# Performance work log

Measured on AMD Instinct MI355X. Metric: run time of the kernel, lower is better.

Reference implementation:

```python
import jax, jax.numpy as jnp
import numpy as np

B, NF, L, DEPTH = 128, 1781, 2048, 4
DI, DS, DC, DTR = 8, 32, 4, 1  # d_inner=expand*d_model, d_state, d_conv, dt_rank


def setup_inputs() -> dict:
    key = jax.random.key(0)
    ks = jax.random.split(key, 32)
    n = lambda k, s, sc=0.02: jax.random.normal(k, s, jnp.float32) * sc
    inp = {
        'x': jax.random.normal(ks[0], (B, NF), jnp.float32),
        # projection1: ReLU -> Linear(NF,2048) -> LayerNorm(2048)
        'p1_W': n(ks[1], (L, NF)), 'p1_b': jnp.zeros((L,), jnp.float32),
        'ln1_g': jnp.ones((L,), jnp.float32), 'ln1_b': jnp.zeros((L,), jnp.float32),
        # per-block Mamba params stacked over depth
        'in_W': n(ks[2], (DEPTH, 2 * DI, 1)),
        'conv_w': n(ks[3], (DEPTH, DI, 1, DC), 0.2),
        'conv_b': jnp.zeros((DEPTH, DI), jnp.float32),
        'xp_W': n(ks[4], (DEPTH, DTR + 2 * DS, DI)),
        'dt_W': n(ks[5], (DEPTH, DI, DTR), 0.5),
        'dt_b': n(ks[6], (DEPTH, DI), 0.5) - 4.0,
        'A_log': jnp.log(jnp.tile(jnp.arange(1, DS + 1, dtype=jnp.float32), (DEPTH, DI, 1))),
        'Dp': jnp.ones((DEPTH, DI), jnp.float32),
        'out_W': n(ks[7], (DEPTH, 1, DI)),
        'rms_w': jnp.ones((DEPTH, 1), jnp.float32),
        # projection2: Linear(2048,512) -> LayerNorm(512) -> ReLU -> Linear(512,256)
        'p2a_W': n(ks[8], (512, L)), 'p2a_b': jnp.zeros((512,), jnp.float32),
        'ln2_g': jnp.ones((512,), jnp.float32), 'ln2_b': jnp.zeros((512,), jnp.float32),
        'p2b_W': n(ks[9], (256, 512)), 'p2b_b': jnp.zeros((256,), jnp.float32),
    }
    return inp


def _layernorm(x, g, b, eps=1e-5):
    m = x.mean(-1, keepdims=True)
    v = ((x - m) ** 2).mean(-1, keepdims=True)
    return (x - m) * jax.lax.rsqrt(v + eps) * g + b


def _silu(x):
    return x * jax.nn.sigmoid(x)


def _mamba(x, in_W, conv_w, conv_b, xp_W, dt_W, dt_b, A_log, Dp, out_W):
    # x: (B, L, 1)
    xz = x @ in_W.T                      # (B, L, 2*DI)
    xc, z = jnp.split(xz, 2, axis=-1)    # (B, L, DI) each
    # causal depthwise conv over L
    xt = jnp.transpose(xc, (0, 2, 1))    # (B, DI, L)
    xt = jax.lax.conv_general_dilated(xt, conv_w, (1,), [(DC - 1, 0)],
                                      dimension_numbers=('NCH', 'OIH', 'NCH'),
                                      feature_group_count=DI)
    xc = _silu(jnp.transpose(xt, (0, 2, 1)) + conv_b)   # (B, L, DI)
    x_dbl = xc @ xp_W.T                                  # (B, L, DTR+2*DS)
    dt, Bm, Cm = jnp.split(x_dbl, [DTR, DTR + DS], axis=-1)
    dt = jax.nn.softplus(dt @ dt_W.T + dt_b)             # (B, L, DI)
    A = -jnp.exp(A_log)                                  # (DI, DS)
    dA = jnp.exp(dt[..., None] * A)                      # (B, L, DI, DS)
    dBx = dt[..., None] * Bm[:, :, None, :] * xc[..., None]
    def comb(e1, e2):
        a1, b1 = e1
        a2, b2 = e2
        return (a2 * a1, a2 * b1 + b2)
    _, h = jax.lax.associative_scan(comb, (dA, dBx), axis=1)  # h: (B,L,DI,DS)
    y = jnp.einsum('blds,bls->bld', h, Cm) + Dp * xc
    y = y * _silu(z)
    return y @ out_W.T                                   # (B, L, 1)


def reference(x, p1_W, p1_b, ln1_g, ln1_b, in_W, conv_w, conv_b, xp_W, dt_W, dt_b,
              A_log, Dp, out_W, rms_w, p2a_W, p2a_b, ln2_g, ln2_b, p2b_W, p2b_b):
    h = jax.nn.relu(x) @ p1_W.T + p1_b
    h = _layernorm(h, ln1_g, ln1_b)
    h = h[..., None]                      # (B, L, 1)
    for i in range(DEPTH):
        # RMSNorm over last dim (size 1): mean(x^2) == x^2
        rn = h * jax.lax.rsqrt(h * h + 1e-5) * rms_w[i]
        h = _mamba(rn, in_W[i], conv_w[i], conv_b[i], xp_W[i], dt_W[i], dt_b[i],
                   A_log[i], Dp[i], out_W[i]) + h
    h = h[..., 0]
    h2 = h @ p2a_W.T + p2a_b
    h2 = jax.nn.relu(_layernorm(h2, ln2_g, ln2_b))
    return h2 @ p2b_W.T + p2b_b
```

## Files before the change

kernel.cpp:

```cpp
#include <hip/hip_runtime.h>
#include <math.h>

#define B_    128
#define NF_   1781
#define L_    2048
#define DEPTH_ 4
#define DI_   8
#define DS_   32
#define NXD_  65
#define NCC_  8
#define CLL_  256
#define SUB_  32
#define MCL_  64
#define KS1_  8
#define KS3_  8
#define LOG2E_ 1.44269504088896f

typedef unsigned long long ull_t;
union F2U { float2 f; ull_t u; };

__device__ __forceinline__ float silu_f(float x) {
    return x / (1.f + __expf(-x));
}
__device__ __forceinline__ float softplus_f(float x) {
    return fmaxf(x, 0.f) + __logf(1.f + __expf(-fabsf(x)));
}
__device__ __forceinline__ float exp2_fast(float x) {
#if __has_builtin(__builtin_amdgcn_exp2f)
    return __builtin_amdgcn_exp2f(x);
#else
    return __expf(x * 0.6931471805599453f);
#endif
}

#define DPP_ADD(x, ctrl)                                                      \
    (x) += __int_as_float(__builtin_amdgcn_update_dpp(                        \
        0, __float_as_int(x), (ctrl), 0xf, 0xf, true))

__device__ __forceinline__ float dpp_sum32_tail(float x) {
    DPP_ADD(x, 0x111);
    DPP_ADD(x, 0x112);
    DPP_ADD(x, 0x114);
    DPP_ADD(x, 0x118);
    DPP_ADD(x, 0x142);
    return x;
}

__device__ __forceinline__ float wave_sum64(float v) {
    v += __shfl_xor(v, 32); v += __shfl_xor(v, 16); v += __shfl_xor(v, 8);
    v += __shfl_xor(v, 4);  v += __shfl_xor(v, 2);  v += __shfl_xor(v, 1);
    return v;
}

__device__ __forceinline__ float block_sum256(float v, float* red) {
    v = wave_sum64(v);
    int tid = threadIdx.x;
    __syncthreads();
    if ((tid & 63) == 0) red[tid >> 6] = v;
    __syncthreads();
    return red[0] + red[1] + red[2] + red[3];
}

__global__ __launch_bounds__(256) void kZero(float4* __restrict__ p) {
    p[blockIdx.x * 256 + threadIdx.x] = make_float4(0.f, 0.f, 0.f, 0.f);
}

__global__ __launch_bounds__(256) void kZeroCtl(unsigned int* __restrict__ p,
                                                int n) {
    int i = blockIdx.x * 256 + threadIdx.x;
    if (i < n) p[i] = 0u;
}

__global__ __launch_bounds__(256) void k1_gemm(const float* __restrict__ x,
                                               const float* __restrict__ W,
                                               float* __restrict__ g1) {
    __shared__ float As[32][36];
    __shared__ float Bs[32][65];
    const int n0 = blockIdx.x * 64, m0 = blockIdx.y * 32;
    const int kb = blockIdx.z * 224;
    const int tid = threadIdx.x;
    const int tn = tid & 63, tm = tid >> 6;
    float acc[8] = {0.f, 0.f, 0.f, 0.f, 0.f, 0.f, 0.f, 0.f};
#pragma unroll 1
    for (int t = 0; t < 7; ++t) {
        const int k0 = kb + t * 32;
#pragma unroll
        for (int j = 0; j < 4; ++j) {
            int idx = tid + 256 * j, k = idx & 31, m = idx >> 5;
            int kk = k0 + k;
            float v = (kk < NF_) ? x[(m0 + m) * NF_ + kk] : 0.f;
            As[k][m] = fmaxf(v, 0.f);
        }
#pragma unroll
        for (int j = 0; j < 8; ++j) {
            int idx = tid + 256 * j, k = idx & 31, n = idx >> 5;
            int kk = k0 + k;
            Bs[k][n] = (kk < NF_) ? W[(size_t)(n0 + n) * NF_ + kk] : 0.f;
        }
        __syncthreads();
#pragma unroll
        for (int k = 0; k < 32; ++k) {
            float4 a0 = *(const float4*)&As[k][tm * 8];
            float4 a1 = *(const float4*)&As[k][tm * 8 + 4];
            float b0 = Bs[k][tn];
            acc[0] = fmaf(a0.x, b0, acc[0]); acc[1] = fmaf(a0.y, b0, acc[1]);
            acc[2] = fmaf(a0.z, b0, acc[2]); acc[3] = fmaf(a0.w, b0, acc[3]);
            acc[4] = fmaf(a1.x, b0, acc[4]); acc[5] = fmaf(a1.y, b0, acc[5]);
            acc[6] = fmaf(a1.z, b0, acc[6]); acc[7] = fmaf(a1.w, b0, acc[7]);
        }
        __syncthreads();
    }
#pragma unroll
    for (int r = 0; r < 8; ++r)
        atomicAdd(&g1[(m0 + tm * 8 + r) * L_ + n0 + tn], acc[r]);
}

__global__ __launch_bounds__(256) void kLN(float* __restrict__ hg,
                                           const float* __restrict__ bias,
                                           const float* __restrict__ g,
                                           const float* __restrict__ bt) {
    __shared__ float red[4];
    const int tid = threadIdx.x;
    float* h = hg + blockIdx.x * L_;
    float s = 0.f;
    for (int l = tid; l < L_; l += 256) s += h[l] + bias[l];
    s = block_sum256(s, red);
    const float mean = s * (1.f / (float)L_);
    float vs = 0.f;
    for (int l = tid; l < L_; l += 256) {
        float d = h[l] + bias[l] - mean; vs += d * d;
    }
    vs = block_sum256(vs, red);
    const float rstd = rsqrtf(vs * (1.f / (float)L_) + 1e-5f);
    for (int l = tid; l < L_; l += 256)
        h[l] = (h[l] + bias[l] - mean) * rstd * g[l] + bt[l];
}

__global__ __launch_bounds__(256) void kS(int dep,
    float* __restrict__ hg, ull_t* __restrict__ PSa,
    unsigned int* __restrict__ ctl,
    const float* __restrict__ in_W,  const float* __restrict__ conv_w,
    const float* __restrict__ conv_b,const float* __restrict__ xp_W,
    const float* __restrict__ dt_W,  const float* __restrict__ dt_b,
    const float* __restrict__ A_log, const float* __restrict__ Dp,
    const float* __restrict__ out_W, const float* __restrict__ rms_w) {
    __shared__ float rnb[CLL_ + 3];
    __shared__ float Pp[88];
    __shared__ float xcvb[CLL_ * 8];
    __shared__ float dtS[CLL_ * 8];
    __shared__ float2 bufA[(SUB_ / 2) * 32];
    __shared__ float2 bufB[(SUB_ / 2) * 32];
    __shared__ float ypartS[SUB_ * 9];
    __shared__ int svid;
    unsigned int* flags  = ctl;
    unsigned int* ticket = ctl + B_ * NCC_;
    const int tid = threadIdx.x;
    if (tid == 0) svid = (int)atomicAdd(&ticket[dep], 1u);
    __syncthreads();
    const int vid = svid;
    const int b = vid >> 3, c = vid & (NCC_ - 1);
    const int c0 = c * CLL_;

    {
        const float rmsw = rms_w[dep];
        for (int i = tid; i < CLL_ + 3; i += 256) {
            int lg = c0 - 3 + i;
            float hv = (lg >= 0) ? hg[(size_t)b * L_ + lg] : 0.f;
            rnb[i] = (lg >= 0) ? hv * rsqrtf(hv * hv + 1e-5f) * rmsw : 0.f;
        }
        if (tid < 88) {
            int t2 = tid;
            Pp[t2] = (t2 < 32)  ? conv_w[dep * 32 + t2]
                   : (t2 < 40)  ? conv_b[dep * 8 + t2 - 32]
                   : (t2 < 56)  ? in_W[dep * 16 + t2 - 40]
                   : (t2 < 64)  ? dt_W[dep * 8 + t2 - 56]
                   : (t2 < 72)  ? dt_b[dep * 8 + t2 - 64]
                   : (t2 < 80)  ? Dp[dep * 8 + t2 - 72]
                                : out_W[dep * 8 + t2 - 80];
        }
    }
    __syncthreads();

    {
        const int dd = tid & 7, lb = tid >> 3;
        const float cw0 = Pp[dd * 4], cw1 = Pp[dd * 4 + 1];
        const float cw2 = Pp[dd * 4 + 2], cw3 = Pp[dd * 4 + 3];
        const float inw = Pp[40 + dd], cb = Pp[32 + dd];
        const float xp0d = xp_W[dep * (NXD_ * 8) + dd];
        const float dtw = Pp[56 + dd], dtb = Pp[64 + dd];
#pragma unroll
        for (int jj = 0; jj < CLL_ / 32; ++jj) {
            int l = lb + 32 * jj;
            float sc = cw0 * rnb[l] + cw1 * rnb[l + 1] +
                       cw2 * rnb[l + 2] + cw3 * rnb[l + 3];
            float v = silu_f(inw * sc + cb);
            xcvb[l * 8 + dd] = v;
            float p = v * xp0d;
            DPP_ADD(p, 0x111); DPP_ADD(p, 0x112); DPP_ADD(p, 0x114);
            float dtraw = __shfl(p, tid | 7);
            dtS[l * 8 + dd] = softplus_f(dtraw * dtw + dtb);
        }
    }
    __syncthreads();

    const int d = tid >> 5, s = tid & 31;
    const int wave = tid >> 6, lane = tid & 63;
    const int kk = lane & 31, half = lane >> 5;
    const float AthL2 = -__expf(A_log[(dep * 8 + d) * 32 + s]) * LOG2E_;

    const float4* wpB = (const float4*)(xp_W + dep * (NXD_ * 8) + (kk + 1) * 8);
    const float4 wBa = wpB[0], wBb = wpB[1];
#define GEMV_B(t, buf)                                                        \
    {                                                                         \
        _Pragma("unroll")                                                     \
        for (int i = 0; i < 4; ++i) {                                         \
            int lsub = wave * 8 + half * 4 + i;                               \
            int l = (t) * SUB_ + lsub;                                        \
            float4 xa = *(const float4*)&xcvb[l * 8];                         \
            float4 xb = *(const float4*)&xcvb[l * 8 + 4];                     \
            float dot = xa.x * wBa.x + xa.y * wBa.y + xa.z * wBa.z +          \
                        xa.w * wBa.w + xb.x * wBb.x + xb.y * wBb.y +          \
                        xb.z * wBb.z + xb.w * wBb.w;                          \
            ((float*)&(buf)[(lsub >> 1) * 32 + kk])[lsub & 1] = dot;          \
        }                                                                     \
    }

    float hloc = 0.f, sdt = 0.f;
    GEMV_B(0, bufA)
    __syncthreads();
#pragma unroll 1
    for (int t = 0; t < CLL_ / SUB_; ++t) {
        if (t + 1 < CLL_ / SUB_) {
            if (t & 1) { GEMV_B(t + 1, bufA) } else { GEMV_B(t + 1, bufB) }
        }
        const float2* cur = (t & 1) ? bufB : bufA;
#pragma unroll
        for (int l2 = 0; l2 < SUB_ / 2; ++l2) {
            float2 bm = cur[l2 * 32 + s];
            int l = t * SUB_ + l2 * 2;
            float dtl = dtS[l * 8 + d];
            float dA = exp2_fast(dtl * AthL2);
            hloc = fmaf(dA, hloc, dtl * xcvb[l * 8 + d] * bm.x);
            sdt += dtl;
            dtl = dtS[(l + 1) * 8 + d];
            dA = exp2_fast(dtl * AthL2);
            hloc = fmaf(dA, hloc, dtl * xcvb[(l + 1) * 8 + d] * bm.y);
            sdt += dtl;
        }
        __syncthreads();
    }
    const float cp = exp2_fast(sdt * AthL2);

    const unsigned int want = (unsigned int)(dep + 1);
    if (c < NCC_ - 1) {
        F2U ou; ou.f = make_float2(cp, hloc);
        __hip_atomic_store(&PSa[((size_t)vid << 8) + tid], ou.u,
                           __ATOMIC_RELAXED, __HIP_MEMORY_SCOPE_AGENT);
    }
    __syncthreads();
    if (c < NCC_ - 1 && tid == 0)
        __hip_atomic_store(&flags[vid], want, __ATOMIC_RELAXED,
                           __HIP_MEMORY_SCOPE_AGENT);

    float h_in = 0.f;
    if (c > 0) {
        if (tid < c) {
            while (__hip_atomic_load(&flags[vid - c + tid], __ATOMIC_RELAXED,
                                     __HIP_MEMORY_SCOPE_AGENT) != want)
                __builtin_amdgcn_s_sleep(4);
        }
        __syncthreads();
        const ull_t* base = PSa + (((size_t)(vid - c)) << 8) + tid;
        ull_t tmp[NCC_ - 1];
#pragma unroll
        for (int j = 0; j < NCC_ - 1; ++j)
            if (j < c)
                tmp[j] = __hip_atomic_load(base + ((size_t)j << 8),
                                           __ATOMIC_RELAXED,
                                           __HIP_MEMORY_SCOPE_AGENT);
#pragma unroll
        for (int j = 0; j < NCC_ - 1; ++j)
            if (j < c) {
                F2U pu; pu.u = tmp[j];
                h_in = fmaf(pu.f.x, h_in, pu.f.y);
            }
    }

    const float4* wpC = (const float4*)(xp_W + dep * (NXD_ * 8) + (lane + 1) * 8);
    const float4 wCa = wpC[0], wCb = wpC[1];
#define GEMV_BC(t)                                                            \
    {                                                                         \
        _Pragma("unroll")                                                     \
        for (int i = 0; i < 8; ++i) {                                         \
            int lsub = wave * 8 + i;                                          \
            int l = (t) * SUB_ + lsub;                                        \
            float4 xa = *(const float4*)&xcvb[l * 8];                         \
            float4 xb = *(const float4*)&xcvb[l * 8 + 4];                     \
            float dot = xa.x * wCa.x + xa.y * wCa.y + xa.z * wCa.z +          \
                        xa.w * wCa.w + xb.x * wCb.x + xb.y * wCb.y +          \
                        xb.z * wCb.z + xb.w * wCb.w;                          \
            if (lane < 32)                                                    \
                ((float*)&bufA[(lsub >> 1) * 32 + kk])[lsub & 1] = dot;       \
            else                                                              \
                ((float*)&bufB[(lsub >> 1) * 32 + kk])[lsub & 1] = dot;       \
        }                                                                     \
    }

#define EPI(t)                                                                \
    if (tid < SUB_) {                                                         \
        int lg = (t) * SUB_ + tid;                                            \
        const float rv = rnb[3 + lg];                                         \
        float o = 0.f;                                                        \
        _Pragma("unroll")                                                     \
        for (int d2 = 0; d2 < 8; ++d2) {                                      \
            float wz = silu_f(rv * Pp[48 + d2]) * Pp[80 + d2];                \
            o += wz * (ypartS[tid * 9 + d2] +                                 \
                       Pp[72 + d2] * xcvb[lg * 8 + d2]);                      \
        }                                                                     \
        hg[(size_t)b * L_ + c0 + lg] += o;                                    \
    }

    float hst = h_in;
#pragma unroll 1
    for (int t = 0; t < CLL_ / SUB_; ++t) {
        GEMV_BC(t)
        if (t > 0) { EPI(t - 1) }
        __syncthreads();
#pragma unroll
        for (int l4 = 0; l4 < SUB_ / 4; ++l4) {
            int lbase = t * SUB_ + l4 * 4;
            float2 bm0 = bufA[(l4 * 2) * 32 + s];
            float2 bm1 = bufA[(l4 * 2 + 1) * 32 + s];
            float2 cm0 = bufB[(l4 * 2) * 32 + s];
            float2 cm1 = bufB[(l4 * 2 + 1) * 32 + s];
            float cr[4];
            float dtl = dtS[lbase * 8 + d];
            float dA = exp2_fast(dtl * AthL2);
            hst = fmaf(dA, hst, dtl * xcvb[lbase * 8 + d] * bm0.x);
            cr[0] = hst * cm0.x;
            dtl = dtS[(lbase + 1) * 8 + d];
            dA = exp2_fast(dtl * AthL2);
            hst = fmaf(dA, hst, dtl * xcvb[(lbase + 1) * 8 + d] * bm0.y);
            cr[1] = hst * cm0.y;
            dtl = dtS[(lbase + 2) * 8 + d];
            dA = exp2_fast(dtl * AthL2);
            hst = fmaf(dA, hst, dtl * xcvb[(lbase + 2) * 8 + d] * bm1.x);
            cr[2] = hst * cm1.x;
            dtl = dtS[(lbase + 3) * 8 + d];
            dA = exp2_fast(dtl * AthL2);
            hst = fmaf(dA, hst, dtl * xcvb[(lbase + 3) * 8 + d] * bm1.y);
            cr[3] = hst * cm1.y;
#pragma unroll
            for (int q = 0; q < 4; ++q) cr[q] = dpp_sum32_tail(cr[q]);
            if ((tid & 31) == 31) {
#pragma unroll
                for (int q = 0; q < 4; ++q)
                    ypartS[(l4 * 4 + q) * 9 + d] = cr[q];
            }
        }
        __syncthreads();
    }
    EPI(CLL_ / SUB_ - 1)
#undef GEMV_B
#undef GEMV_BC
#undef EPI
}

__global__ __launch_bounds__(256) void k3_gemm(const float* __restrict__ h,
                                               const float* __restrict__ W,
                                               float* __restrict__ part) {
    __shared__ float As[32][20];
    __shared__ float Bs[32][65];
    const int n0 = blockIdx.x * 64, m0 = blockIdx.y * 16;
    const int kb = blockIdx.z * 256;
    const int tid = threadIdx.x;
    const int tn = tid & 63, tm = tid >> 6;
    float acc[4] = {0.f, 0.f, 0.f, 0.f};
#pragma unroll 1
    for (int t = 0; t < 8; ++t) {
        const int k0 = kb + t * 32;
#pragma unroll
        for (int j = 0; j < 2; ++j) {
            int idx = tid + 256 * j, k = idx & 31, m = idx >> 5;
            As[k][m] = h[(m0 + m) * L_ + k0 + k];
        }
#pragma unroll
        for (int j = 0; j < 8; ++j) {
            int idx = tid + 256 * j, k = idx & 31, n = idx >> 5;
            Bs[k][n] = W[(size_t)(n0 + n) * L_ + k0 + k];
        }
        __syncthreads();
#pragma unroll
        for (int k = 0; k < 32; ++k) {
            float4 a = *(const float4*)&As[k][tm * 4];
            float b0 = Bs[k][tn];
            acc[0] = fmaf(a.x, b0, acc[0]);
            acc[1] = fmaf(a.y, b0, acc[1]);
            acc[2] = fmaf(a.z, b0, acc[2]);
            acc[3] = fmaf(a.w, b0, acc[3]);
        }
        __syncthreads();
    }
    float* pp = part + (size_t)blockIdx.z * (B_ * 512);
#pragma unroll
    for (int r = 0; r < 4; ++r)
        pp[(m0 + tm * 4 + r) * 512 + n0 + tn] = acc[r];
}

__global__ __launch_bounds__(256) void k4_head(const float* __restrict__ part,
    const float* __restrict__ b1,
    const float* __restrict__ g,  const float* __restrict__ bt,
    const float* __restrict__ W2, const float* __restrict__ b2,
    float* __restrict__ out) {
    __shared__ alignas(16) float t2r[512];
    __shared__ alignas(16) float y2[512];
    __shared__ float red[4];
    const int m = blockIdx.x, tid = threadIdx.x;
#pragma unroll
    for (int j = 0; j < 2; ++j) {
        const int n = tid + 256 * j;
        float v = b1[n];
#pragma unroll
        for (int ks = 0; ks < KS3_; ++ks)
            v += part[(size_t)ks * (B_ * 512) + m * 512 + n];
        t2r[n] = v;
    }
    __syncthreads();
    float v0 = t2r[tid], v1 = t2r[tid + 256];
    float s = block_sum256(v0 + v1, red);
    float mean = s * (1.f / 512.f);
    float d0 = v0 - mean, d1 = v1 - mean;
    float var = block_sum256(d0 * d0 + d1 * d1, red) * (1.f / 512.f);
    float rs = rsqrtf(var + 1e-5f);
    y2[tid]       = fmaxf(d0 * rs * g[tid] + bt[tid], 0.f);
    y2[tid + 256] = fmaxf(d1 * rs * g[tid + 256] + bt[tid + 256], 0.f);
    __syncthreads();
    float acc = b2[tid];
    const float* wr = W2 + tid * 512;
    for (int j = 0; j < 512; j += 4) {
        float4 w4 = *(const float4*)&wr[j];
        float4 yv = *(const float4*)&y2[j];
        acc = fmaf(w4.x, yv.x, acc); acc = fmaf(w4.y, yv.y, acc);
        acc = fmaf(w4.z, yv.z, acc); acc = fmaf(w4.w, yv.w, acc);
    }
    out[m * 256 + tid] = acc;
}

struct MambaLds {
    float P_in[16], P_cw[32], P_cb[8], P_dtw[8], P_dtb[8], P_dp[8], P_ow[8];
    alignas(16) float P_xp[NXD_ * 8];
    float rnb[L_ + 3];
    alignas(16) float xcvb[MCL_ * 8];
    alignas(16) float BmS[MCL_ * 33];
    alignas(16) float CmS[MCL_ * 33];
    float2 dtuS[MCL_ * 8];
    float dtrawS[MCL_], offS[MCL_];
    float ypartS[MCL_ * 8];
    float red[4];
};

__device__ void head_body(const float* hrow, float* t2r, float* y2, float* red,
    const float* __restrict__ W1, const float* __restrict__ b1,
    const float* __restrict__ g,  const float* __restrict__ bt,
    const float* __restrict__ W2, const float* __restrict__ b2,
    float* __restrict__ outrow) {
    const int tid = threadIdx.x, wave = tid >> 6, lane = tid & 63;
    for (int i = 0; i < 128; ++i) {
        const int n = wave * 128 + i;
        const float* wr = W1 + (size_t)n * L_;
        float acc = 0.f;
        for (int k0 = lane * 4; k0 < L_; k0 += 256) {
            float4 w4 = *(const float4*)&wr[k0];
            float4 hv = *(const float4*)&hrow[k0];
            acc = fmaf(w4.x, hv.x, acc); acc = fmaf(w4.y, hv.y, acc);
            acc = fmaf(w4.z, hv.z, acc); acc = fmaf(w4.w, hv.w, acc);
        }
        acc = wave_sum64(acc);
        if (lane == 0) t2r[n] = acc + b1[n];
    }
    __syncthreads();
    float v0 = t2r[tid], v1 = t2r[tid + 256];
    float s = block_sum256(v0 + v1, red);
    float mean = s * (1.f / 512.f);
    float d0 = v0 - mean, d1 = v1 - mean;
    float var = block_sum256(d0 * d0 + d1 * d1, red) * (1.f / 512.f);
    float rs = rsqrtf(var + 1e-5f);
    y2[tid]       = fmaxf(d0 * rs * g[tid] + bt[tid], 0.f);
    y2[tid + 256] = fmaxf(d1 * rs * g[tid + 256] + bt[tid + 256], 0.f);
    __syncthreads();
    for (int i = 0; i < 64; ++i) {
        const int n = wave * 64 + i;
        const float* wr = W2 + n * 512;
        float acc = 0.f;
        for (int k0 = lane * 4; k0 < 512; k0 += 256) {
            float4 w4 = *(const float4*)&wr[k0];
            float4 yv = *(const float4*)&y2[k0];
            acc = fmaf(w4.x, yv.x, acc); acc = fmaf(w4.y, yv.y, acc);
            acc = fmaf(w4.z, yv.z, acc); acc = fmaf(w4.w, yv.w, acc);
        }
        acc = wave_sum64(acc);
        if (lane == 0) outrow[n] = acc + b2[n];
    }
}

__device__ void mamba_body(float* h, MambaLds& S,
    const float* __restrict__ ln1_g, const float* __restrict__ ln1_b,
    const float* __restrict__ in_W,  const float* __restrict__ conv_w,
    const float* __restrict__ conv_b,const float* __restrict__ xp_W,
    const float* __restrict__ dt_W,  const float* __restrict__ dt_b,
    const float* __restrict__ A_log, const float* __restrict__ Dp,
    const float* __restrict__ out_W, const float* __restrict__ rms_w) {
    const int tid = threadIdx.x;
    float s = 0.f;
    for (int l = tid; l < L_; l += 256) s += h[l];
    s = block_sum256(s, S.red);
    const float mean = s * (1.f / (float)L_);
    float vs = 0.f;
    for (int l = tid; l < L_; l += 256) { float d = h[l] - mean; vs += d * d; }
    vs = block_sum256(vs, S.red);
    const float rstd = rsqrtf(vs * (1.f / (float)L_) + 1e-5f);
    for (int l = tid; l < L_; l += 256)
        h[l] = (h[l] - mean) * rstd * ln1_g[l] + ln1_b[l];
    __syncthreads();
    const int dd_s = tid >> 5, ss_s = tid & 31;
    for (int dep = 0; dep < DEPTH_; ++dep) {
        if (tid < 16) S.P_in[tid] = in_W[dep * 16 + tid];
        if (tid >= 32 && tid < 64) S.P_cw[tid - 32] = conv_w[dep * 32 + (tid - 32)];
        if (tid >= 64 && tid < 72) S.P_cb[tid - 64] = conv_b[dep * 8 + (tid - 64)];
        if (tid >= 72 && tid < 80) S.P_dtw[tid - 72] = dt_W[dep * 8 + (tid - 72)];
        if (tid >= 80 && tid < 88) S.P_dtb[tid - 80] = dt_b[dep * 8 + (tid - 80)];
        if (tid >= 88 && tid < 96) S.P_dp[tid - 88] = Dp[dep * 8 + (tid - 88)];
        if (tid >= 96 && tid < 104) S.P_ow[tid - 96] = out_W[dep * 8 + (tid - 96)];
        for (int j = tid; j < NXD_ * 8; j += 256) S.P_xp[j] = xp_W[dep * NXD_ * 8 + j];
        const float rmsw = rms_w[dep];
        const float Ath = -__expf(A_log[(dep * 8 + dd_s) * 32 + ss_s]);
        if (tid < 3) S.rnb[tid] = 0.f;
        __syncthreads();
        for (int l = tid; l < L_; l += 256) {
            float hv = h[l];
            S.rnb[3 + l] = hv * rsqrtf(hv * hv + 1e-5f) * rmsw;
        }
        __syncthreads();
        float hst = 0.f;
        for (int c0 = 0; c0 < L_; c0 += MCL_) {
            {
                const int dd = tid & 7, lb = tid >> 3;
                const float cw0 = S.P_cw[dd * 4 + 0], cw1 = S.P_cw[dd * 4 + 1];
                const float cw2 = S.P_cw[dd * 4 + 2], cw3 = S.P_cw[dd * 4 + 3];
                const float inw = S.P_in[dd], cb = S.P_cb[dd];
#pragma unroll
                for (int j = 0; j < MCL_ / 32; ++j) {
                    int l = lb + 32 * j, lg = c0 + l;
                    float sc = cw0 * S.rnb[lg] + cw1 * S.rnb[lg + 1] +
                               cw2 * S.rnb[lg + 2] + cw3 * S.rnb[lg + 3];
                    S.xcvb[l * 8 + dd] = silu_f(inw * sc + cb);
                }
            }
            __syncthreads();
            {
                const int l = tid & 63, q = tid >> 6;
                const float4 xa = *(const float4*)&S.xcvb[l * 8];
                const float4 xb = *(const float4*)&S.xcvb[l * 8 + 4];
                const int j0 = (q == 0) ? 0 : (17 + (q - 1) * 16);
                const int j1 = 17 + q * 16;
                for (int j = j0; j < j1; ++j) {
                    const float4 wa = *(const float4*)&S.P_xp[j * 8];
                    const float4 wb = *(const float4*)&S.P_xp[j * 8 + 4];
                    float dot = xa.x * wa.x + xa.y * wa.y + xa.z * wa.z + xa.w * wa.w +
                                xb.x * wb.x + xb.y * wb.y + xb.z * wb.z + xb.w * wb.w;
                    if (j == 0)      S.dtrawS[l] = dot;
                    else if (j < 33) S.BmS[l * 33 + (j - 1)] = dot;
                    else             S.CmS[l * 33 + (j - 33)] = dot;
                }
            }
            __syncthreads();
            {
                const int dd = tid & 7, lb = tid >> 3;
                const float dtw = S.P_dtw[dd], dtbv = S.P_dtb[dd];
#pragma unroll
                for (int j = 0; j < MCL_ / 32; ++j) {
                    int l = lb + 32 * j;
                    float dt = softplus_f(S.dtrawS[l] * dtw + dtbv);
                    float xcv = S.xcvb[l * 8 + dd];
                    S.dtuS[l * 8 + dd] = make_float2(dt, dt * xcv);
                }
            }
            if (tid < MCL_) {
                const int l = tid;
                const float rv = S.rnb[3 + c0 + l];
                float o = 0.f;
#pragma unroll
                for (int d2 = 0; d2 < 8; ++d2) {
                    float wz = silu_f(rv * S.P_in[8 + d2]) * S.P_ow[d2];
                    o += wz * S.P_dp[d2] * S.xcvb[l * 8 + d2];
                }
                S.offS[l] = o;
            }
            __syncthreads();
#pragma unroll 4
            for (int l = 0; l < MCL_; ++l) {
                float2 du = S.dtuS[l * 8 + dd_s];
                float Bv = S.BmS[l * 33 + ss_s];
                float Cv = S.CmS[l * 33 + ss_s];
                float dA = __expf(du.x * Ath);
                hst = fmaf(dA, hst, du.y * Bv);
                float c = dpp_sum32_tail(hst * Cv);
                if ((tid & 31) == 31) S.ypartS[l * 8 + dd_s] = c;
            }
            __syncthreads();
            if (tid < MCL_) {
                const int l = tid, lg = c0 + l;
                const float rv = S.rnb[3 + lg];
                float o = S.offS[l];
#pragma unroll
                for (int d2 = 0; d2 < 8; ++d2) {
                    float wz = silu_f(rv * S.P_in[8 + d2]) * S.P_ow[d2];
                    o += wz * S.ypartS[l * 8 + d2];
                }
                h[lg] += o;
            }
            __syncthreads();
        }
        __syncthreads();
    }
}

__global__ __launch_bounds__(256) void mega(
    const float* __restrict__ x,
    const float* __restrict__ p1_W, const float* __restrict__ p1_b,
    const float* __restrict__ ln1_g, const float* __restrict__ ln1_b,
    const float* __restrict__ in_W, const float* __restrict__ conv_w,
    const float* __restrict__ conv_b, const float* __restrict__ xp_W,
    const float* __restrict__ dt_W, const float* __restrict__ dt_b,
    const float* __restrict__ A_log, const float* __restrict__ Dp,
    const float* __restrict__ out_W, const float* __restrict__ rms_w,
    const float* __restrict__ p2a_W, const float* __restrict__ p2a_b,
    const float* __restrict__ ln2_g, const float* __restrict__ ln2_b,
    const float* __restrict__ p2b_W, const float* __restrict__ p2b_b,
    float* __restrict__ out) {
    __shared__ alignas(16) float hrow[L_];
    __shared__ MambaLds S;
    const int b = blockIdx.x, tid = threadIdx.x, wave = tid >> 6, lane = tid & 63;
    float* xrow = (float*)S.BmS;
    for (int k = tid; k < 1792; k += 256)
        xrow[k] = (k < NF_) ? fmaxf(x[b * NF_ + k], 0.f) : 0.f;
    __syncthreads();
    for (int i = 0; i < 512; ++i) {
        const int l = wave * 512 + i;
        const float* wr = p1_W + (size_t)l * NF_;
        float acc = 0.f;
        for (int k0 = lane * 4; k0 < NF_; k0 += 256) {
            if (k0 + 3 < NF_) {
                float4 w4 = *(const float4*)&wr[k0];
                float4 xv = *(const float4*)&xrow[k0];
                acc = fmaf(w4.x, xv.x, acc); acc = fmaf(w4.y, xv.y, acc);
                acc = fmaf(w4.z, xv.z, acc); acc = fmaf(w4.w, xv.w, acc);
            } else {
                for (int c = 0; c < 4; ++c)
                    if (k0 + c < NF_) acc = fmaf(wr[k0 + c], xrow[k0 + c], acc);
            }
        }
        acc = wave_sum64(acc);
        if (lane == 0) hrow[l] = acc + p1_b[l];
    }
    __syncthreads();
    mamba_body((float*)hrow, S, ln1_g, ln1_b, in_W, conv_w, conv_b,
               xp_W, dt_W, dt_b, A_log, Dp, out_W, rms_w);
    float* t2r = (float*)S.BmS;
    float* y2  = (float*)S.CmS;
    head_body((const float*)hrow, t2r, y2, S.red, p2a_W, p2a_b,
              ln2_g, ln2_b, p2b_W, p2b_b, out + b * 256);
}

extern "C" void kernel_launch(void* const* d_in, const int* in_sizes, int n_in,
                              void* d_out, int out_size, void* d_ws, size_t ws_size,
                              hipStream_t stream) {
    const float* x     = (const float*)d_in[0];
    const float* p1_W  = (const float*)d_in[1];
    const float* p1_b  = (const float*)d_in[2];
    const float* ln1_g = (const float*)d_in[3];
    const float* ln1_b = (const float*)d_in[4];
    const float* in_W  = (const float*)d_in[5];
    const float* conv_w= (const float*)d_in[6];
    const float* conv_b= (const float*)d_in[7];
    const float* xp_W  = (const float*)d_in[8];
    const float* dt_W  = (const float*)d_in[9];
    const float* dt_b  = (const float*)d_in[10];
    const float* A_log = (const float*)d_in[11];
    const float* Dp    = (const float*)d_in[12];
    const float* out_W = (const float*)d_in[13];
    const float* rms_w = (const float*)d_in[14];
    const float* p2a_W = (const float*)d_in[15];
    const float* p2a_b = (const float*)d_in[16];
    const float* ln2_g = (const float*)d_in[17];
    const float* ln2_b = (const float*)d_in[18];
    const float* p2b_W = (const float*)d_in[19];
    const float* p2b_b = (const float*)d_in[20];
    float* o = (float*)d_out;

    const size_t need = (size_t)B_ * L_ * sizeof(float);
    if (ws_size >= need) {
        float* h = (float*)d_ws;
        float* scr = (float*)d_in[1];
        ull_t* PSa = (ull_t*)scr;
        unsigned int* ctl = (unsigned int*)(scr + (size_t)B_ * NCC_ * 256 * 2);
        float* t2p = scr;

        kZero<<<L_ * B_ / 1024, 256, 0, stream>>>((float4*)h);
        dim3 grd1(L_ / 64, B_ / 32, KS1_);
        k1_gemm<<<grd1, 256, 0, stream>>>(x, p1_W, h);
        kZeroCtl<<<(B_ * NCC_ + DEPTH_ + 255) / 256, 256, 0, stream>>>(
            ctl, B_ * NCC_ + DEPTH_);
        kLN<<<B_, 256, 0, stream>>>(h, p1_b, ln1_g, ln1_b);
        for (int dep = 0; dep < DEPTH_; ++dep) {
            kS<<<dim3(B_ * NCC_), 256, 0, stream>>>(dep, h, PSa, ctl,
                                                    in_W, conv_w, conv_b, xp_W,
                                                    dt_W, dt_b, A_log, Dp,
                                                    out_W, rms_w);
        }
        dim3 grd3(512 / 64, B_ / 16, KS3_);
        k3_gemm<<<grd3, 256, 0, stream>>>(h, p2a_W, t2p);
        k4_head<<<B_, 256, 0, stream>>>(t2p, p2a_b, ln2_g, ln2_b,
                                        p2b_W, p2b_b, o);
    } else {
        mega<<<B_, 256, 0, stream>>>(x, p1_W, p1_b, ln1_g, ln1_b, in_W, conv_w,
                                     conv_b, xp_W, dt_W, dt_b, A_log, Dp, out_W,
                                     rms_w, p2a_W, p2a_b, ln2_g, ln2_b,
                                     p2b_W, p2b_b, o);
    }
}
```

Measured before the change: 471.1 us.

## Fuse four Mamba depth launches into one persistent kernel with halo exchange

Replaces the four per-depth scan kernel launches with a single kernel that loops over depth. Each chunk keeps its slice of the residual stream in shared memory, and only the 3-element conv halo goes through global memory to the next chunk, guarded by per-depth flags. This removes three launches, the global read-modify-write of h at every depth, and the wait at each kernel boundary, so chunks can move on to the next depth as soon as their left neighbour is ready. In exchange it needs more scratch space for per-depth prefix states and halos, and it relies on the ticket ordering to keep inter-block spin waits free of deadlock.

```diff
diff --git a/kernel.cpp b/kernel.cpp
--- a/kernel.cpp
+++ b/kernel.cpp
@@ -10,6 +10,7 @@
 #define NXD_  65
 #define NCC_  8
 #define CLL_  256
+#define NVID_ (B_ * NCC_)
 #define SUB_  32
 #define MCL_  64
 #define KS1_  8
@@ -136,14 +137,15 @@
         h[l] = (h[l] + bias[l] - mean) * rstd * g[l] + bt[l];
 }
 
-__global__ __launch_bounds__(256) void kS(int dep,
+__global__ __launch_bounds__(256) void kSF(
     float* __restrict__ hg, ull_t* __restrict__ PSa,
-    unsigned int* __restrict__ ctl,
+    float* __restrict__ halo, unsigned int* __restrict__ ctl,
     const float* __restrict__ in_W,  const float* __restrict__ conv_w,
     const float* __restrict__ conv_b,const float* __restrict__ xp_W,
     const float* __restrict__ dt_W,  const float* __restrict__ dt_b,
     const float* __restrict__ A_log, const float* __restrict__ Dp,
     const float* __restrict__ out_W, const float* __restrict__ rms_w) {
+    __shared__ float hS[CLL_];
     __shared__ float rnb[CLL_ + 3];
     __shared__ float Pp[88];
     __shared__ float xcvb[CLL_ * 8];
@@ -153,20 +155,49 @@
     __shared__ float ypartS[SUB_ * 9];
     __shared__ int svid;
     unsigned int* flags  = ctl;
-    unsigned int* ticket = ctl + B_ * NCC_;
+    unsigned int* eflags = ctl + NVID_;
+    unsigned int* ticket = ctl + 2 * NVID_;
     const int tid = threadIdx.x;
-    if (tid == 0) svid = (int)atomicAdd(&ticket[dep], 1u);
+    if (tid == 0) svid = (int)atomicAdd(ticket, 1u);
     __syncthreads();
     const int vid = svid;
     const int b = vid >> 3, c = vid & (NCC_ - 1);
     const int c0 = c * CLL_;
-
-    {
+    const int d = tid >> 5, s = tid & 31;
+    const int wave = tid >> 6, lane = tid & 63;
+    const int kk = lane & 31, half = lane >> 5;
+
+#pragma unroll 1
+    for (int dep = 0; dep < DEPTH_; ++dep) {
         const float rmsw = rms_w[dep];
-        for (int i = tid; i < CLL_ + 3; i += 256) {
-            int lg = c0 - 3 + i;
-            float hv = (lg >= 0) ? hg[(size_t)b * L_ + lg] : 0.f;
-            rnb[i] = (lg >= 0) ? hv * rsqrtf(hv * hv + 1e-5f) * rmsw : 0.f;
+        if (dep == 0) {
+            float hv = hg[(size_t)b * L_ + c0 + tid];
+            hS[tid] = hv;
+            rnb[3 + tid] = hv * rsqrtf(hv * hv + 1e-5f) * rmsw;
+            if (tid < 3) {
+                int lg = c0 - 3 + tid;
+                float h2 = (lg >= 0) ? hg[(size_t)b * L_ + lg] : 0.f;
+                rnb[tid] = (lg >= 0) ? h2 * rsqrtf(h2 * h2 + 1e-5f) * rmsw : 0.f;
+            }
+        } else {
+            if (c > 0 && tid == 0) {
+                while (__hip_atomic_load(&eflags[vid - 1], __ATOMIC_RELAXED,
+                                         __HIP_MEMORY_SCOPE_AGENT) <
+                       (unsigned)dep)
+                    __builtin_amdgcn_s_sleep(4);
+            }
+            __syncthreads();
+            float hv = hS[tid];
+            rnb[3 + tid] = hv * rsqrtf(hv * hv + 1e-5f) * rmsw;
+            if (tid < 3) {
+                float h2 = 0.f;
+                if (c > 0)
+                    h2 = __hip_atomic_load(
+                        &halo[(size_t)(dep - 1) * (NVID_ * 4) +
+                              (size_t)(vid - 1) * 4 + tid],
+                        __ATOMIC_RELAXED, __HIP_MEMORY_SCOPE_AGENT);
+                rnb[tid] = (c > 0) ? h2 * rsqrtf(h2 * h2 + 1e-5f) * rmsw : 0.f;
+            }
         }
         if (tid < 88) {
             int t2 = tid;
@@ -178,38 +209,35 @@
                    : (t2 < 80)  ? Dp[dep * 8 + t2 - 72]
                                 : out_W[dep * 8 + t2 - 80];
         }
-    }
-    __syncthreads();
-
-    {
-        const int dd = tid & 7, lb = tid >> 3;
-        const float cw0 = Pp[dd * 4], cw1 = Pp[dd * 4 + 1];
-        const float cw2 = Pp[dd * 4 + 2], cw3 = Pp[dd * 4 + 3];
-        const float inw = Pp[40 + dd], cb = Pp[32 + dd];
-        const float xp0d = xp_W[dep * (NXD_ * 8) + dd];
-        const float dtw = Pp[56 + dd], dtb = Pp[64 + dd];
-#pragma unroll
-        for (int jj = 0; jj < CLL_ / 32; ++jj) {
-            int l = lb + 32 * jj;
-            float sc = cw0 * rnb[l] + cw1 * rnb[l + 1] +
-                       cw2 * rnb[l + 2] + cw3 * rnb[l + 3];
-            float v = silu_f(inw * sc + cb);
-            xcvb[l * 8 + dd] = v;
-            float p = v * xp0d;
-            DPP_ADD(p, 0x111); DPP_ADD(p, 0x112); DPP_ADD(p, 0x114);
-            float dtraw = __shfl(p, tid | 7);
-            dtS[l * 8 + dd] = softplus_f(dtraw * dtw + dtb);
-        }
-    }
-    __syncthreads();
-
-    const int d = tid >> 5, s = tid & 31;
-    const int wave = tid >> 6, lane = tid & 63;
-    const int kk = lane & 31, half = lane >> 5;
-    const float AthL2 = -__expf(A_log[(dep * 8 + d) * 32 + s]) * LOG2E_;
-
-    const float4* wpB = (const float4*)(xp_W + dep * (NXD_ * 8) + (kk + 1) * 8);
-    const float4 wBa = wpB[0], wBb = wpB[1];
+        __syncthreads();
+
+        {
+            const int dd = tid & 7, lb = tid >> 3;
+            const float cw0 = Pp[dd * 4], cw1 = Pp[dd * 4 + 1];
+            const float cw2 = Pp[dd * 4 + 2], cw3 = Pp[dd * 4 + 3];
+            const float inw = Pp[40 + dd], cb = Pp[32 + dd];
+            const float xp0d = xp_W[dep * (NXD_ * 8) + dd];
+            const float dtw = Pp[56 + dd], dtb = Pp[64 + dd];
+#pragma unroll
+            for (int jj = 0; jj < CLL_ / 32; ++jj) {
+                int l = lb + 32 * jj;
+                float sc = cw0 * rnb[l] + cw1 * rnb[l + 1] +
+                           cw2 * rnb[l + 2] + cw3 * rnb[l + 3];
+                float v = silu_f(inw * sc + cb);
+                xcvb[l * 8 + dd] = v;
+                float p = v * xp0d;
+                DPP_ADD(p, 0x111); DPP_ADD(p, 0x112); DPP_ADD(p, 0x114);
+                float dtraw = __shfl(p, tid | 7);
+                dtS[l * 8 + dd] = softplus_f(dtraw * dtw + dtb);
+            }
+        }
+        __syncthreads();
+
+        const float AthL2 = -__expf(A_log[(dep * 8 + d) * 32 + s]) * LOG2E_;
+
+        const float4* wpB =
+            (const float4*)(xp_W + dep * (NXD_ * 8) + (kk + 1) * 8);
+        const float4 wBa = wpB[0], wBb = wpB[1];
 #define GEMV_B(t, buf)                                                        \
     {                                                                         \
         _Pragma("unroll")                                                     \
@@ -225,69 +253,72 @@
         }                                                                     \
     }
 
-    float hloc = 0.f, sdt = 0.f;
-    GEMV_B(0, bufA)
-    __syncthreads();
+        float hloc = 0.f, sdt = 0.f;
+        GEMV_B(0, bufA)
+        __syncthreads();
 #pragma unroll 1
-    for (int t = 0; t < CLL_ / SUB_; ++t) {
-        if (t + 1 < CLL_ / SUB_) {
-            if (t & 1) { GEMV_B(t + 1, bufA) } else { GEMV_B(t + 1, bufB) }
-        }
-        const float2* cur = (t & 1) ? bufB : bufA;
-#pragma unroll
-        for (int l2 = 0; l2 < SUB_ / 2; ++l2) {
-            float2 bm = cur[l2 * 32 + s];
-            int l = t * SUB_ + l2 * 2;
-            float dtl = dtS[l * 8 + d];
-            float dA = exp2_fast(dtl * AthL2);
-            hloc = fmaf(dA, hloc, dtl * xcvb[l * 8 + d] * bm.x);
-            sdt += dtl;
-            dtl = dtS[(l + 1) * 8 + d];
-            dA = exp2_fast(dtl * AthL2);
-            hloc = fmaf(dA, hloc, dtl * xcvb[(l + 1) * 8 + d] * bm.y);
-            sdt += dtl;
-        }
-        __syncthreads();
-    }
-    const float cp = exp2_fast(sdt * AthL2);
-
-    const unsigned int want = (unsigned int)(dep + 1);
-    if (c < NCC_ - 1) {
-        F2U ou; ou.f = make_float2(cp, hloc);
-        __hip_atomic_store(&PSa[((size_t)vid << 8) + tid], ou.u,
-                           __ATOMIC_RELAXED, __HIP_MEMORY_SCOPE_AGENT);
-    }
-    __syncthreads();
-    if (c < NCC_ - 1 && tid == 0)
-        __hip_atomic_store(&flags[vid], want, __ATOMIC_RELAXED,
-                           __HIP_MEMORY_SCOPE_AGENT);
-
-    float h_in = 0.f;
-    if (c > 0) {
-        if (tid < c) {
-            while (__hip_atomic_load(&flags[vid - c + tid], __ATOMIC_RELAXED,
-                                     __HIP_MEMORY_SCOPE_AGENT) != want)
-                __builtin_amdgcn_s_sleep(4);
-        }
-        __syncthreads();
-        const ull_t* base = PSa + (((size_t)(vid - c)) << 8) + tid;
-        ull_t tmp[NCC_ - 1];
-#pragma unroll
-        for (int j = 0; j < NCC_ - 1; ++j)
-            if (j < c)
-                tmp[j] = __hip_atomic_load(base + ((size_t)j << 8),
-                                           __ATOMIC_RELAXED,
-                                           __HIP_MEMORY_SCOPE_AGENT);
-#pragma unroll
-        for (int j = 0; j < NCC_ - 1; ++j)
-            if (j < c) {
-                F2U pu; pu.u = tmp[j];
-                h_in = fmaf(pu.f.x, h_in, pu.f.y);
-            }
-    }
-
-    const float4* wpC = (const float4*)(xp_W + dep * (NXD_ * 8) + (lane + 1) * 8);
-    const float4 wCa = wpC[0], wCb = wpC[1];
+        for (int t = 0; t < CLL_ / SUB_; ++t) {
+            if (t + 1 < CLL_ / SUB_) {
+                if (t & 1) { GEMV_B(t + 1, bufA) } else { GEMV_B(t + 1, bufB) }
+            }
+            const float2* cur = (t & 1) ? bufB : bufA;
+#pragma unroll
+            for (int l2 = 0; l2 < SUB_ / 2; ++l2) {
+                float2 bm = cur[l2 * 32 + s];
+                int l = t * SUB_ + l2 * 2;
+                float dtl = dtS[l * 8 + d];
+                float dA = exp2_fast(dtl * AthL2);
+                hloc = fmaf(dA, hloc, dtl * xcvb[l * 8 + d] * bm.x);
+                sdt += dtl;
+                dtl = dtS[(l + 1) * 8 + d];
+                dA = exp2_fast(dtl * AthL2);
+                hloc = fmaf(dA, hloc, dtl * xcvb[(l + 1) * 8 + d] * bm.y);
+                sdt += dtl;
+            }
+            __syncthreads();
+        }
+        const float cp = exp2_fast(sdt * AthL2);
+
+        const unsigned int want = (unsigned int)(dep + 1);
+        ull_t* PSd = PSa + (size_t)dep * (NVID_ * 256);
+        if (c < NCC_ - 1) {
+            F2U ou; ou.f = make_float2(cp, hloc);
+            __hip_atomic_store(&PSd[((size_t)vid << 8) + tid], ou.u,
+                               __ATOMIC_RELAXED, __HIP_MEMORY_SCOPE_AGENT);
+        }
+        __syncthreads();
+        if (c < NCC_ - 1 && tid == 0)
+            __hip_atomic_store(&flags[vid], want, __ATOMIC_RELAXED,
+                               __HIP_MEMORY_SCOPE_AGENT);
+
+        float h_in = 0.f;
+        if (c > 0) {
+            if (tid < c) {
+                while (__hip_atomic_load(&flags[vid - c + tid],
+                                         __ATOMIC_RELAXED,
+                                         __HIP_MEMORY_SCOPE_AGENT) < want)
+                    __builtin_amdgcn_s_sleep(4);
+            }
+            __syncthreads();
+            const ull_t* base = PSd + (((size_t)(vid - c)) << 8) + tid;
+            ull_t tmp[NCC_ - 1];
+#pragma unroll
+            for (int j = 0; j < NCC_ - 1; ++j)
+                if (j < c)
+                    tmp[j] = __hip_atomic_load(base + ((size_t)j << 8),
+                                               __ATOMIC_RELAXED,
+                                               __HIP_MEMORY_SCOPE_AGENT);
+#pragma unroll
+            for (int j = 0; j < NCC_ - 1; ++j)
+                if (j < c) {
+                    F2U pu; pu.u = tmp[j];
+                    h_in = fmaf(pu.f.x, h_in, pu.f.y);
+                }
+        }
+
+        const float4* wpC =
+            (const float4*)(xp_W + dep * (NXD_ * 8) + (lane + 1) * 8);
+        const float4 wCa = wpC[0], wCb = wpC[1];
 #define GEMV_BC(t)                                                            \
     {                                                                         \
         _Pragma("unroll")                                                     \
@@ -317,53 +348,67 @@
             o += wz * (ypartS[tid * 9 + d2] +                                 \
                        Pp[72 + d2] * xcvb[lg * 8 + d2]);                      \
         }                                                                     \
-        hg[(size_t)b * L_ + c0 + lg] += o;                                    \
-    }
-
-    float hst = h_in;
+        float hnew = hS[lg] + o;                                              \
+        hS[lg] = hnew;                                                        \
+        if (dep == DEPTH_ - 1) {                                              \
+            hg[(size_t)b * L_ + c0 + lg] = hnew;                              \
+        } else if (c < NCC_ - 1 && lg >= CLL_ - 3) {                          \
+            __hip_atomic_store(&halo[(size_t)dep * (NVID_ * 4) +              \
+                                     (size_t)vid * 4 + (lg - (CLL_ - 3))],    \
+                               hnew, __ATOMIC_RELAXED,                        \
+                               __HIP_MEMORY_SCOPE_AGENT);                     \
+        }                                                                     \
+    }
+
+        float hst = h_in;
 #pragma unroll 1
-    for (int t = 0; t < CLL_ / SUB_; ++t) {
-        GEMV_BC(t)
-        if (t > 0) { EPI(t - 1) }
-        __syncthreads();
-#pragma unroll
-        for (int l4 = 0; l4 < SUB_ / 4; ++l4) {
-            int lbase = t * SUB_ + l4 * 4;
-            float2 bm0 = bufA[(l4 * 2) * 32 + s];
-            float2 bm1 = bufA[(l4 * 2 + 1) * 32 + s];
-            float2 cm0 = bufB[(l4 * 2) * 32 + s];
-            float2 cm1 = bufB[(l4 * 2 + 1) * 32 + s];
-            float cr[4];
-            float dtl = dtS[lbase * 8 + d];
-            float dA = exp2_fast(dtl * AthL2);
-            hst = fmaf(dA, hst, dtl * xcvb[lbase * 8 + d] * bm0.x);
-            cr[0] = hst * cm0.x;
-            dtl = dtS[(lbase + 1) * 8 + d];
-            dA = exp2_fast(dtl * AthL2);
-            hst = fmaf(dA, hst, dtl * xcvb[(lbase + 1) * 8 + d] * bm0.y);
-            cr[1] = hst * cm0.y;
-            dtl = dtS[(lbase + 2) * 8 + d];
-            dA = exp2_fast(dtl * AthL2);
-            hst = fmaf(dA, hst, dtl * xcvb[(lbase + 2) * 8 + d] * bm1.x);
-            cr[2] = hst * cm1.x;
-            dtl = dtS[(lbase + 3) * 8 + d];
-            dA = exp2_fast(dtl * AthL2);
-            hst = fmaf(dA, hst, dtl * xcvb[(lbase + 3) * 8 + d] * bm1.y);
-            cr[3] = hst * cm1.y;
-#pragma unroll
-            for (int q = 0; q < 4; ++q) cr[q] = dpp_sum32_tail(cr[q]);
-            if ((tid & 31) == 31) {
-#pragma unroll
-                for (int q = 0; q < 4; ++q)
-                    ypartS[(l4 * 4 + q) * 9 + d] = cr[q];
-            }
-        }
-        __syncthreads();
-    }
-    EPI(CLL_ / SUB_ - 1)
+        for (int t = 0; t < CLL_ / SUB_; ++t) {
+            GEMV_BC(t)
+            if (t > 0) { EPI(t - 1) }
+            __syncthreads();
+#pragma unroll
+            for (int l4 = 0; l4 < SUB_ / 4; ++l4) {
+                int lbase = t * SUB_ + l4 * 4;
+                float2 bm0 = bufA[(l4 * 2) * 32 + s];
+                float2 bm1 = bufA[(l4 * 2 + 1) * 32 + s];
+                float2 cm0 = bufB[(l4 * 2) * 32 + s];
+                float2 cm1 = bufB[(l4 * 2 + 1) * 32 + s];
+                float cr[4];
+                float dtl = dtS[lbase * 8 + d];
+                float dA = exp2_fast(dtl * AthL2);
+                hst = fmaf(dA, hst, dtl * xcvb[lbase * 8 + d] * bm0.x);
+                cr[0] = hst * cm0.x;
+                dtl = dtS[(lbase + 1) * 8 + d];
+                dA = exp2_fast(dtl * AthL2);
+                hst = fmaf(dA, hst, dtl * xcvb[(lbase + 1) * 8 + d] * bm0.y);
+                cr[1] = hst * cm0.y;
+                dtl = dtS[(lbase + 2) * 8 + d];
+                dA = exp2_fast(dtl * AthL2);
+                hst = fmaf(dA, hst, dtl * xcvb[(lbase + 2) * 8 + d] * bm1.x);
+                cr[2] = hst * cm1.x;
+                dtl = dtS[(lbase + 3) * 8 + d];
+                dA = exp2_fast(dtl * AthL2);
+                hst = fmaf(dA, hst, dtl * xcvb[(lbase + 3) * 8 + d] * bm1.y);
+                cr[3] = hst * cm1.y;
+#pragma unroll
+                for (int q = 0; q < 4; ++q) cr[q] = dpp_sum32_tail(cr[q]);
+                if ((tid & 31) == 31) {
+#pragma unroll
+                    for (int q = 0; q < 4; ++q)
+                        ypartS[(l4 * 4 + q) * 9 + d] = cr[q];
+                }
+            }
+            __syncthreads();
+        }
+        EPI(CLL_ / SUB_ - 1)
+        __syncthreads();
+        if (dep < DEPTH_ - 1 && c < NCC_ - 1 && tid == 0)
+            __hip_atomic_store(&eflags[vid], (unsigned)(dep + 1),
+                               __ATOMIC_RELAXED, __HIP_MEMORY_SCOPE_AGENT);
 #undef GEMV_B
 #undef GEMV_BC
 #undef EPI
+    }
 }
 
 __global__ __launch_bounds__(256) void k3_gemm(const float* __restrict__ h,
@@ -703,21 +748,20 @@
         float* h = (float*)d_ws;
         float* scr = (float*)d_in[1];
         ull_t* PSa = (ull_t*)scr;
-        unsigned int* ctl = (unsigned int*)(scr + (size_t)B_ * NCC_ * 256 * 2);
+        float* halo = scr + (size_t)DEPTH_ * NVID_ * 256 * 2;
+        unsigned int* ctl = (unsigned int*)(halo + DEPTH_ * NVID_ * 4);
         float* t2p = scr;
 
         kZero<<<L_ * B_ / 1024, 256, 0, stream>>>((float4*)h);
         dim3 grd1(L_ / 64, B_ / 32, KS1_);
         k1_gemm<<<grd1, 256, 0, stream>>>(x, p1_W, h);
-        kZeroCtl<<<(B_ * NCC_ + DEPTH_ + 255) / 256, 256, 0, stream>>>(
-            ctl, B_ * NCC_ + DEPTH_);
+        kZeroCtl<<<(2 * NVID_ + 1 + 255) / 256, 256, 0, stream>>>(
+            ctl, 2 * NVID_ + 1);
         kLN<<<B_, 256, 0, stream>>>(h, p1_b, ln1_g, ln1_b);
-        for (int dep = 0; dep < DEPTH_; ++dep) {
-            kS<<<dim3(B_ * NCC_), 256, 0, stream>>>(dep, h, PSa, ctl,
-                                                    in_W, conv_w, conv_b, xp_W,
-                                                    dt_W, dt_b, A_log, Dp,
-                                                    out_W, rms_w);
-        }
+        kSF<<<dim3(NVID_), 256, 0, stream>>>(h, PSa, halo, ctl,
+                                             in_W, conv_w, conv_b, xp_W,
+                                             dt_W, dt_b, A_log, Dp,
+                                             out_W, rms_w);
         dim3 grd3(512 / 64, B_ / 16, KS3_);
         k3_gemm<<<grd3, 256, 0, stream>>>(h, p2a_W, t2p);
         k4_head<<<B_, 256, 0, stream>>>(t2p, p2a_b, ln2_g, ln2_b,
```

Result: slower. 521.7 us (+10.7%).
